# Kernel optimization log

Measured on AMD Instinct MI355X. Metric: run time of the kernel, lower is better.

The kernel has to match this reference:

```python
import jax, jax.numpy as jnp
import numpy as np

N_LAYER = 3
N_HEAD = 12
D_K = 64
D_V = 64
D_MODEL = 768
D_INNER = 4096
LN_EPS = 1e-5
BN_EPS = 1e-5
PAD_ID = 1


def _layernorm(x, g, b):
    m = jnp.mean(x, axis=-1, keepdims=True)
    v = jnp.mean((x - m) ** 2, axis=-1, keepdims=True)
    return g * (x - m) / jnp.sqrt(v + LN_EPS) + b


def _batchnorm(x, g, b):
    # training-mode BatchNorm1d: per-feature batch statistics
    m = jnp.mean(x, axis=0)
    v = jnp.mean((x - m) ** 2, axis=0)
    return g * (x - m) / jnp.sqrt(v + BN_EPS) + b


def setup_inputs() -> dict:
    key = jax.random.key(0)
    ks = jax.random.split(key, 24)
    B, C, S, H = 4, 4, 256, D_MODEL
    inp = {
        'input_ids': jax.random.randint(ks[0], (B, C, S), 0, 50000, dtype=jnp.int64) if jax.config.read('jax_enable_x64') else jax.random.randint(ks[0], (B, C, S), 0, 50000, dtype=jnp.int32),
        'roberta_attn': jax.random.normal(ks[1], (B, C, S, H), dtype=jnp.float32),
        'pooled_output': jax.random.normal(ks[2], (B * C, H), dtype=jnp.float32),
        'commonsense_mask': jax.random.uniform(ks[3], (B, C, S, S), dtype=jnp.float32),
        'dependency_mask': jax.random.uniform(ks[4], (B, C, S, S), dtype=jnp.float32),
        'entity_mask': jax.random.uniform(ks[5], (B, C, S), dtype=jnp.float32),
        'sentiment_mask': jax.random.uniform(ks[6], (B, C, S, S), dtype=jnp.float32),
    }
    s = 0.02
    inp['lin_w'] = s * jax.random.normal(ks[7], (H, N_LAYER * 4), dtype=jnp.float32)
    inp['lin_b'] = jnp.zeros((N_LAYER * 4,), jnp.float32)
    inp['Wq'] = s * jax.random.normal(ks[8], (N_LAYER, H, N_HEAD * D_K), dtype=jnp.float32)
    inp['bq'] = jnp.zeros((N_LAYER, N_HEAD * D_K), jnp.float32)
    inp['Wk'] = s * jax.random.normal(ks[9], (N_LAYER, H, N_HEAD * D_K), dtype=jnp.float32)
    inp['bk'] = jnp.zeros((N_LAYER, N_HEAD * D_K), jnp.float32)
    inp['Wv'] = s * jax.random.normal(ks[10], (N_LAYER, H, N_HEAD * D_V), dtype=jnp.float32)
    inp['bv'] = jnp.zeros((N_LAYER, N_HEAD * D_V), jnp.float32)
    inp['Wo'] = s * jax.random.normal(ks[11], (N_LAYER, N_HEAD * D_V, H), dtype=jnp.float32)
    inp['bo'] = jnp.zeros((N_LAYER, H), jnp.float32)
    inp['ln1_g'] = jnp.ones((N_LAYER, H), jnp.float32)
    inp['ln1_b'] = jnp.zeros((N_LAYER, H), jnp.float32)
    inp['W1'] = s * jax.random.normal(ks[12], (N_LAYER, H, D_INNER), dtype=jnp.float32)
    inp['b1'] = jnp.zeros((N_LAYER, D_INNER), jnp.float32)
    inp['W2'] = s * jax.random.normal(ks[13], (N_LAYER, D_INNER, H), dtype=jnp.float32)
    inp['b2'] = jnp.zeros((N_LAYER, H), jnp.float32)
    inp['ln2_g'] = jnp.ones((N_LAYER, H), jnp.float32)
    inp['ln2_b'] = jnp.zeros((N_LAYER, H), jnp.float32)
    inp['bnt_g'] = jnp.ones((H,), jnp.float32)
    inp['bnt_b'] = jnp.zeros((H,), jnp.float32)
    inp['pool_w'] = s * jax.random.normal(ks[14], (H, H), dtype=jnp.float32)
    inp['pool_b'] = jnp.zeros((H,), jnp.float32)
    inp['bn_g'] = jnp.ones((H,), jnp.float32)
    inp['bn_b'] = jnp.zeros((H,), jnp.float32)
    inp['cls_w'] = s * jax.random.normal(ks[15], (H, 1), dtype=jnp.float32)
    inp['cls_b'] = jnp.zeros((1,), jnp.float32)
    return inp


def reference(input_ids, roberta_attn, pooled_output, commonsense_mask, dependency_mask,
              entity_mask, sentiment_mask, lin_w, lin_b, Wq, bq, Wk, bk, Wv, bv, Wo, bo,
              ln1_g, ln1_b, W1, b1, W2, b2, ln2_g, ln2_b, bnt_g, bnt_b,
              pool_w, pool_b, bn_g, bn_b, cls_w, cls_b):
    B, C, S = input_ids.shape
    H = roberta_attn.shape[-1]
    N = B * C
    x = roberta_attn.reshape(N, S, H)

    # learned softmax fusion weights over the 4 relational masks, per layer
    w = jnp.mean(x, axis=1) @ lin_w + lin_b                       # [N, 3*4]
    w = jax.nn.softmax(w.reshape(N, N_LAYER, 4).transpose(1, 0, 2), axis=-1)  # [3, N, 4]

    ent = jnp.broadcast_to(entity_mask[:, :, None, :], (B, C, S, S))
    masks = jnp.stack([
        commonsense_mask.reshape(N, S, S),
        dependency_mask.reshape(N, S, S),
        ent.reshape(N, S, S),
        sentiment_mask.reshape(N, S, S),
    ], axis=1)                                                     # [N, 4, S, S]
    bias = jnp.einsum('lnm,nmqk->lnqk', w, masks)                  # [3, N, S, S]

    non_pad = (input_ids.reshape(N, S) != PAD_ID).astype(x.dtype)[:, :, None]  # [N, S, 1]

    enc = x
    scale = 1.0 / np.sqrt(D_K).astype(np.float32)
    for l in range(N_LAYER):
        residual = enc
        q = (enc @ Wq[l] + bq[l]).reshape(N, S, N_HEAD, D_K)
        k = (enc @ Wk[l] + bk[l]).reshape(N, S, N_HEAD, D_K)
        v = (enc @ Wv[l] + bv[l]).reshape(N, S, N_HEAD, D_V)
        scores = jnp.einsum('nqhd,nkhd->nhqk', q, k) * scale + bias[l][:, None]  # [N,H,S,S]
        attn = jax.nn.softmax(scores, axis=-1)
        o = jnp.einsum('nhqk,nkhd->nqhd', attn, v).reshape(N, S, N_HEAD * D_V)
        o = o @ Wo[l] + bo[l]
        enc = _layernorm(o + residual, ln1_g[l], ln1_b[l]) * non_pad
        residual = enc
        f = jax.nn.relu(enc @ W1[l] + b1[l]) @ W2[l] + b2[l]
        enc = _layernorm(f + residual, ln2_g[l], ln2_b[l]) * non_pad

    enc = _batchnorm(enc.reshape(N * S, H), bnt_g, bnt_b).reshape(N, S, H)
    seq = x + enc
    pooled = jnp.tanh(seq[:, 0] @ pool_w + pool_b)
    pooled = _batchnorm(pooled, bn_g, bn_b)
    logits = pooled @ cls_w + cls_b                                # [N, 1]
    return logits.reshape(-1, C)
```

## Files before the change

### kernel.cpp

```cpp
#include <hip/hip_runtime.h>
#include <hip/hip_bf16.h>
#include <math.h>

#define NSEQ 16
#define SEQ 256
#define H 768
#define NH 12
#define DKH 64
#define DI 4096
#define MROWS (NSEQ*SEQ)
#define QKVN (3*H)

typedef __bf16 v8bf __attribute__((ext_vector_type(8)));
typedef float  v4f  __attribute__((ext_vector_type(4)));
typedef short  v8s  __attribute__((ext_vector_type(8)));

__device__ inline unsigned short bf16b(float f) {
  __hip_bfloat16 h = __float2bfloat16(f);
  return *reinterpret_cast<unsigned short*>(&h);
}
__device__ inline float b2f(unsigned short b) {
  return __uint_as_float(((unsigned int)b) << 16);
}

__device__ __forceinline__ void gload16(const void* g, void* l) {
  __builtin_amdgcn_global_load_lds((const __attribute__((address_space(1))) void*)g,
                                   (__attribute__((address_space(3))) void*)l, 16, 0, 0);
}

__device__ __forceinline__ void waitvm(int n) {
  switch (n) {
    case 0:  asm volatile("s_waitcnt vmcnt(0)" ::: "memory"); break;
    case 4:  asm volatile("s_waitcnt vmcnt(4)" ::: "memory"); break;
    case 8:  asm volatile("s_waitcnt vmcnt(8)" ::: "memory"); break;
    case 12: asm volatile("s_waitcnt vmcnt(12)" ::: "memory"); break;
    case 16: asm volatile("s_waitcnt vmcnt(16)" ::: "memory"); break;
    default: asm volatile("s_waitcnt vmcnt(0)" ::: "memory"); break;
  }
}

enum { MODE_F32_BIAS=0, MODE_BF16_BIAS=1, MODE_BF16_BIAS_RELU=2, MODE_SCORES=3, MODE_PV=4, MODE_F32_NOBIAS=5 };

template<int BM, int BN, int MODE, int DEPTH, bool SWZ>
__global__ __launch_bounds__(256) void k_mm(
    const unsigned short* __restrict__ A, int lda, long long saN, long long saH,
    const unsigned short* __restrict__ B, int ldb, long long sbN, long long sbH,
    void* __restrict__ Cout, int ldc, long long scN, long long scH,
    const float* __restrict__ bias, int K, int nhdiv) {
  constexpr int MI = BM/32, NI = BN/32;
  constexpr int AISS = BM/32, BISS = BN/32;
  constexpr int LPT = AISS + BISS;
  constexpr int TA = BM*64, TB = BN*64;
  __shared__ unsigned short As[DEPTH*TA];
  __shared__ unsigned short Bs[DEPTH*TB];
  int t = threadIdx.x;
  int z = blockIdx.z, n = z / nhdiv, h = z - n*nhdiv;
  int lane = t & 63, wid = t >> 6, wr = wid >> 1, wc = wid & 1;

  int bx = blockIdx.x, by = blockIdx.y;
  if (SWZ) {
    int gx = gridDim.x;
    int nwg = gx * gridDim.y;
    int lin = by*gx + bx;
    int q = nwg >> 3, r = nwg & 7;
    int xcd = lin & 7, idx = lin >> 3;
    int swz = (xcd < r) ? (xcd*(q+1) + idx) : (r*(q+1) + (xcd-r)*q + idx);
    bx = swz % gx; by = swz / gx;
  }

  const unsigned short* Ab = A + (size_t)n*saN + (size_t)h*saH + (size_t)by*BM*lda;
  const unsigned short* Bb = B + (size_t)n*sbN + (size_t)h*sbH + (size_t)bx*BN*ldb;

  const unsigned short* aSrc[AISS]; int aOff[AISS];
#pragma unroll
  for (int r = 0; r < AISS; ++r) {
    int chunk = wid*AISS + r;
    int row = chunk*8 + (lane >> 3);
    int col = ((lane & 7) ^ (row & 7)) * 8;
    aSrc[r] = Ab + (size_t)row*lda + col;
    aOff[r] = chunk*512;
  }
  const unsigned short* bSrc[BISS]; int bOff[BISS];
#pragma unroll
  for (int r = 0; r < BISS; ++r) {
    int chunk = wid*BISS + r;
    int row = chunk*8 + (lane >> 3);
    int col = ((lane & 7) ^ (row & 7)) * 8;
    bSrc[r] = Bb + (size_t)row*ldb + col;
    bOff[r] = chunk*512;
  }

  v4f acc[MI][NI];
#pragma unroll
  for (int i = 0; i < MI; ++i)
#pragma unroll
    for (int j = 0; j < NI; ++j) acc[i][j] = (v4f){0.f,0.f,0.f,0.f};

  auto issue = [&](int tt, int buf) {
    int k0 = tt << 6;
#pragma unroll
    for (int r = 0; r < AISS; ++r) gload16(aSrc[r] + k0, &As[buf*TA + aOff[r]]);
#pragma unroll
    for (int r = 0; r < BISS; ++r) gload16(bSrc[r] + k0, &Bs[buf*TB + bOff[r]]);
  };

  int nt = K >> 6;
  for (int p = 0; p < DEPTH-1 && p < nt; ++p) issue(p, p);
  int cbuf = 0;
  int ibuf = (DEPTH-1) % DEPTH;
  for (int tt = 0; tt < nt; ++tt) {
    int ahead = tt + DEPTH - 1;
    if (ahead < nt) {
      issue(ahead, ibuf);
      waitvm((DEPTH-1)*LPT);
    } else {
      waitvm((nt-1-tt)*LPT);
    }
    __builtin_amdgcn_s_barrier();
    asm volatile("" ::: "memory");
#pragma unroll
    for (int ks = 0; ks < 2; ++ks) {
      v8bf af[MI], bfr[NI];
#pragma unroll
      for (int i = 0; i < MI; ++i) {
        int row = wr*(BM/2) + i*16 + (lane & 15);
        int c = (ks*4 + (lane >> 4)) ^ (row & 7);
        af[i] = *(const v8bf*)&As[cbuf*TA + row*64 + c*8];
      }
#pragma unroll
      for (int j = 0; j < NI; ++j) {
        int row = wc*(BN/2) + j*16 + (lane & 15);
        int c = (ks*4 + (lane >> 4)) ^ (row & 7);
        bfr[j] = *(const v8bf*)&Bs[cbuf*TB + row*64 + c*8];
      }
#pragma unroll
      for (int i = 0; i < MI; ++i)
#pragma unroll
        for (int j = 0; j < NI; ++j)
          acc[i][j] = __builtin_amdgcn_mfma_f32_16x16x32_bf16(af[i], bfr[j], acc[i][j], 0, 0, 0);
    }
    asm volatile("s_waitcnt lgkmcnt(0)" ::: "memory");
    __builtin_amdgcn_s_barrier();
    asm volatile("" ::: "memory");
    cbuf = (cbuf + 1 == DEPTH) ? 0 : cbuf + 1;
    ibuf = (ibuf + 1 == DEPTH) ? 0 : ibuf + 1;
  }

  float* Cf = (float*)Cout;
  unsigned short* Ch = (unsigned short*)Cout;
  size_t cb = (size_t)n*scN + (size_t)h*scH;
  int grow0 = by*BM + wr*(BM/2);
  int gcol0 = bx*BN + wc*(BN/2);
#pragma unroll
  for (int i = 0; i < MI; ++i) {
#pragma unroll
    for (int j = 0; j < NI; ++j) {
      int col = gcol0 + j*16 + (lane & 15);
      float bval = 0.f;
      if (MODE == MODE_F32_BIAS || MODE == MODE_BF16_BIAS || MODE == MODE_BF16_BIAS_RELU)
        bval = bias[col];
#pragma unroll
      for (int r = 0; r < 4; ++r) {
        int row = grow0 + i*16 + (lane>>4)*4 + r;
        float v = acc[i][j][r];
        if (MODE == MODE_F32_BIAS) {
          Cf[cb + (size_t)row*ldc + col] = v + bval;
        } else if (MODE == MODE_F32_NOBIAS) {
          Cf[cb + (size_t)row*ldc + col] = v;
        } else if (MODE == MODE_PV) {
          Ch[cb + (size_t)row*ldc + col] = bf16b(v);
        } else {
          v += bval;
          if (MODE == MODE_BF16_BIAS_RELU) v = fmaxf(v, 0.f);
          Ch[cb + (size_t)row*ldc + col] = bf16b(v);
        }
      }
    }
  }
}

template<int MODE>
__global__ __launch_bounds__(512) void k_mm256(
    const unsigned short* __restrict__ A, int lda,
    const unsigned short* __restrict__ B, int ldb,
    void* __restrict__ Cout, int ldc,
    const float* __restrict__ bias, int K) {
  extern __shared__ __align__(16) unsigned short smem[];
  unsigned short* As = smem;
  unsigned short* Bs = smem + 2*16384;
  constexpr int TA = 256*64;
  int t = threadIdx.x, lane = t & 63, wid = t >> 6;
  int wr = wid >> 2, wc = wid & 3;

  int bx = blockIdx.x, by = blockIdx.y;
  {
    int gx = gridDim.x, nwg = gx * gridDim.y;
    int lin = by*gx + bx;
    int q = nwg >> 3, r = nwg & 7;
    int xcd = lin & 7, idx = lin >> 3;
    int swz = (xcd < r) ? (xcd*(q+1) + idx) : (r*(q+1) + (xcd-r)*q + idx);
    bx = swz % gx; by = swz / gx;
  }

  const unsigned short* Ab = A + (size_t)by*256*lda;
  const unsigned short* Bb = B + (size_t)bx*256*ldb;

  const unsigned short* aSrc[4]; int aOff[4];
  const unsigned short* bSrc[4]; int bOff[4];
#pragma unroll
  for (int r = 0; r < 4; ++r) {
    int chunk = wid*4 + r;
    int row = chunk*8 + (lane >> 3);
    int col = ((lane & 7) ^ (row & 7)) * 8;
    aSrc[r] = Ab + (size_t)row*lda + col;
    bSrc[r] = Bb + (size_t)row*ldb + col;
    aOff[r] = chunk*512;
    bOff[r] = chunk*512;
  }

  v4f acc[8][4];
#pragma unroll
  for (int i = 0; i < 8; ++i)
#pragma unroll
    for (int j = 0; j < 4; ++j) acc[i][j] = (v4f){0.f,0.f,0.f,0.f};

  auto issue = [&](int tt, int buf) {
    int k0 = tt << 6;
#pragma unroll
    for (int r = 0; r < 4; ++r) gload16(aSrc[r] + k0, &As[buf*TA + aOff[r]]);
#pragma unroll
    for (int r = 0; r < 4; ++r) gload16(bSrc[r] + k0, &Bs[buf*TA + bOff[r]]);
  };

  int nt = K >> 6;
  issue(0, 0);
  int cur = 0;
  for (int tt = 0; tt < nt; ++tt) {
    if (tt + 1 < nt) {
      issue(tt+1, cur^1);
      waitvm(8);
    } else {
      waitvm(0);
    }
    __builtin_amdgcn_s_barrier();
    asm volatile("" ::: "memory");
    __builtin_amdgcn_s_setprio(1);
#pragma unroll
    for (int ks = 0; ks < 2; ++ks) {
      v8bf af[8], bfr[4];
#pragma unroll
      for (int i = 0; i < 8; ++i) {
        int row = wr*128 + i*16 + (lane & 15);
        int c = (ks*4 + (lane >> 4)) ^ (row & 7);
        af[i] = *(const v8bf*)&As[cur*TA + row*64 + c*8];
      }
#pragma unroll
      for (int j = 0; j < 4; ++j) {
        int row = wc*64 + j*16 + (lane & 15);
        int c = (ks*4 + (lane >> 4)) ^ (row & 7);
        bfr[j] = *(const v8bf*)&Bs[cur*TA + row*64 + c*8];
      }
#pragma unroll
      for (int i = 0; i < 8; ++i)
#pragma unroll
        for (int j = 0; j < 4; ++j)
          acc[i][j] = __builtin_amdgcn_mfma_f32_16x16x32_bf16(af[i], bfr[j], acc[i][j], 0, 0, 0);
    }
    __builtin_amdgcn_s_setprio(0);
    asm volatile("s_waitcnt lgkmcnt(0)" ::: "memory");
    __builtin_amdgcn_s_barrier();
    asm volatile("" ::: "memory");
    cur ^= 1;
  }

  float* Cf = (float*)Cout;
  unsigned short* Ch = (unsigned short*)Cout;
  int grow0 = by*256 + wr*128;
  int gcol0 = bx*256 + wc*64;
#pragma unroll
  for (int i = 0; i < 8; ++i) {
#pragma unroll
    for (int j = 0; j < 4; ++j) {
      int col = gcol0 + j*16 + (lane & 15);
      float bval = 0.f;
      if (MODE == MODE_F32_BIAS || MODE == MODE_BF16_BIAS || MODE == MODE_BF16_BIAS_RELU)
        bval = bias[col];
#pragma unroll
      for (int r = 0; r < 4; ++r) {
        int row = grow0 + i*16 + (lane>>4)*4 + r;
        float v = acc[i][j][r];
        if (MODE == MODE_F32_BIAS) {
          Cf[(size_t)row*ldc + col] = v + bval;
        } else if (MODE == MODE_F32_NOBIAS) {
          Cf[(size_t)row*ldc + col] = v;
        } else {
          v += bval;
          if (MODE == MODE_BF16_BIAS_RELU) v = fmaxf(v, 0.f);
          Ch[(size_t)row*ldc + col] = bf16b(v);
        }
      }
    }
  }
}

__global__ __launch_bounds__(256) void k_qksm(
    const unsigned short* __restrict__ qkv,
    const float* __restrict__ biasb,
    unsigned short* __restrict__ P) {
  __shared__ unsigned short Qs[64*64];
  __shared__ unsigned short Ks[256*64];
  int t = threadIdx.x, lane = t & 63, wid = t >> 6;
  int z = blockIdx.y, n = z / NH, h = z - n*NH;
  int m0 = blockIdx.x * 64;
  const unsigned short* Qb = qkv + (size_t)n*SEQ*QKVN + (size_t)h*DKH + (size_t)m0*QKVN;
  const unsigned short* Kb = qkv + (size_t)n*SEQ*QKVN + H + (size_t)h*DKH;
#pragma unroll
  for (int r = 0; r < 2; ++r) {
    int chunk = wid*2 + r;
    int row = chunk*8 + (lane >> 3);
    int col = ((lane & 7) ^ (row & 7)) * 8;
    gload16(Qb + (size_t)row*QKVN + col, &Qs[chunk*512]);
  }
#pragma unroll
  for (int r = 0; r < 8; ++r) {
    int chunk = wid*8 + r;
    int row = chunk*8 + (lane >> 3);
    int col = ((lane & 7) ^ (row & 7)) * 8;
    gload16(Kb + (size_t)row*QKVN + col, &Ks[chunk*512]);
  }
  __syncthreads();
  v4f acc[16];
#pragma unroll
  for (int j = 0; j < 16; ++j) acc[j] = (v4f){0.f,0.f,0.f,0.f};
#pragma unroll
  for (int ks = 0; ks < 2; ++ks) {
    int arow = wid*16 + (lane & 15);
    int ac = (ks*4 + (lane >> 4)) ^ (arow & 7);
    v8bf af = *(const v8bf*)&Qs[arow*64 + ac*8];
#pragma unroll
    for (int j = 0; j < 16; ++j) {
      int brow = j*16 + (lane & 15);
      int bc = (ks*4 + (lane >> 4)) ^ (brow & 7);
      v8bf bf = *(const v8bf*)&Ks[brow*64 + bc*8];
      acc[j] = __builtin_amdgcn_mfma_f32_16x16x32_bf16(af, bf, acc[j], 0, 0, 0);
    }
  }
  int col = lane & 15, quad = lane >> 4;
  const float* bb = biasb + (size_t)n*65536;
  float e[16][4];
  float rm[4] = {-1e30f, -1e30f, -1e30f, -1e30f};
#pragma unroll
  for (int r = 0; r < 4; ++r) {
    int row = m0 + wid*16 + quad*4 + r;
#pragma unroll
    for (int j = 0; j < 16; ++j) {
      float v = acc[j][r]*0.125f + bb[(size_t)row*256 + j*16 + col];
      e[j][r] = v;
      rm[r] = fmaxf(rm[r], v);
    }
  }
#pragma unroll
  for (int r = 0; r < 4; ++r)
#pragma unroll
    for (int m = 1; m < 16; m <<= 1) rm[r] = fmaxf(rm[r], __shfl_xor(rm[r], m, 64));
  float rs[4] = {0.f, 0.f, 0.f, 0.f};
#pragma unroll
  for (int r = 0; r < 4; ++r)
#pragma unroll
    for (int j = 0; j < 16; ++j) {
      float ev = __expf(e[j][r] - rm[r]);
      e[j][r] = ev;
      rs[r] += ev;
    }
#pragma unroll
  for (int r = 0; r < 4; ++r) {
#pragma unroll
    for (int m = 1; m < 16; m <<= 1) rs[r] += __shfl_xor(rs[r], m, 64);
    rs[r] = 1.0f/rs[r];
  }
  unsigned short* Pz = P + (size_t)z*65536;
#pragma unroll
  for (int r = 0; r < 4; ++r) {
    int row = m0 + wid*16 + quad*4 + r;
#pragma unroll
    for (int j = 0; j < 16; ++j)
      Pz[(size_t)row*256 + j*16 + col] = bf16b(e[j][r]*rs[r]);
  }
}

__global__ __launch_bounds__(256) void k_wT(const float* __restrict__ in,
                                            unsigned short* __restrict__ out,
                                            int Nn, int Kk) {
  int n0 = blockIdx.x*64, k0 = blockIdx.y*64;
  __shared__ float T[64][72];
  int t = threadIdx.x;
  int r = t >> 4, c4 = (t & 15) * 4;
#pragma unroll
  for (int i = 0; i < 4; ++i) {
    float4 v = *(const float4*)(in + (size_t)(k0 + r + i*16)*Nn + n0 + c4);
    T[c4+0][r+i*16] = v.x; T[c4+1][r+i*16] = v.y;
    T[c4+2][r+i*16] = v.z; T[c4+3][r+i*16] = v.w;
  }
  __syncthreads();
  int c = t >> 3, r8 = (t & 7) * 8;
#pragma unroll
  for (int i = 0; i < 2; ++i) {
    int cc = c + i*32;
    v8s o;
#pragma unroll
    for (int j = 0; j < 8; ++j) o[j] = (short)bf16b(T[cc][r8+j]);
    *(v8s*)(out + (size_t)(n0+cc)*Kk + k0 + r8) = o;
  }
}

__global__ void k_bqkv(const float* __restrict__ bq, const float* __restrict__ bk,
                       const float* __restrict__ bv, float* __restrict__ o) {
  int i = blockIdx.x*256 + threadIdx.x;
  if (i >= 3*QKVN) return;
  int l = i / QKVN, j = i - l*QKVN;
  float v = (j < H) ? bq[l*H + j] : (j < 2*H) ? bk[l*H + j - H] : bv[l*H + j - 2*H];
  o[i] = v;
}

__global__ __launch_bounds__(256) void k_cast(const float* __restrict__ x,
                                              float* __restrict__ enc,
                                              unsigned short* __restrict__ enc16) {
  size_t i = ((size_t)blockIdx.x*256 + threadIdx.x)*4;
  float4 v = *(const float4*)(x + i);
  *(float4*)(enc + i) = v;
  ushort4 u = { bf16b(v.x), bf16b(v.y), bf16b(v.z), bf16b(v.w) };
  *(ushort4*)(enc16 + i) = u;
}

__global__ __launch_bounds__(256) void k_vT(const unsigned short* __restrict__ qkv,
                                            unsigned short* __restrict__ vT) {
  int z = blockIdx.x, n = z/NH, h = z - n*NH;
  const unsigned short* src = qkv + (size_t)n*SEQ*QKVN + 2*H + (size_t)h*DKH;
  __shared__ unsigned short tile[64][264];
  int t = threadIdx.x;
  int r0 = t >> 3, d0 = (t & 7) * 8;
#pragma unroll
  for (int i = 0; i < 8; ++i) {
    int r = r0 + i*32;
    v8s vv = *(const v8s*)(src + (size_t)r*QKVN + d0);
#pragma unroll
    for (int j = 0; j < 8; ++j) tile[d0+j][r] = (unsigned short)vv[j];
  }
  __syncthreads();
  int d = t >> 2, rb = (t & 3) * 64;
  unsigned short* dst = vT + (size_t)z*DKH*SEQ + (size_t)d*SEQ + rb;
#pragma unroll
  for (int i = 0; i < 8; ++i)
    *(v8s*)(dst + i*8) = *(const v8s*)&tile[d][rb + i*8];
}

__global__ __launch_bounds__(256) void k_fusion_weights(
    const float* __restrict__ x, const float* __restrict__ lin_w,
    const float* __restrict__ lin_b, float* __restrict__ wsoft) {
  int n = blockIdx.x, t = threadIdx.x;
  __shared__ float xm[H];
  __shared__ float sred[4];
  __shared__ float logits[12];
  if (t < 192) {
    const float4* p = (const float4*)(x + (size_t)n*SEQ*H) + t;
    float4 s = {0.f,0.f,0.f,0.f};
    for (int r = 0; r < SEQ; ++r) {
      float4 v = p[(size_t)r*192];
      s.x += v.x; s.y += v.y; s.z += v.z; s.w += v.w;
    }
    xm[t*4+0] = s.x*(1.0f/SEQ); xm[t*4+1] = s.y*(1.0f/SEQ);
    xm[t*4+2] = s.z*(1.0f/SEQ); xm[t*4+3] = s.w*(1.0f/SEQ);
  }
  __syncthreads();
  float lacc[12];
#pragma unroll
  for (int j = 0; j < 12; ++j) lacc[j] = 0.f;
  for (int hh = t; hh < H; hh += 256) {
    float xv = xm[hh];
#pragma unroll
    for (int j = 0; j < 12; ++j) lacc[j] += xv * lin_w[hh*12 + j];
  }
  for (int j = 0; j < 12; ++j) {
    float v = lacc[j];
#pragma unroll
    for (int m = 1; m < 64; m <<= 1) v += __shfl_xor(v, m, 64);
    if ((t & 63) == 0) sred[t >> 6] = v;
    __syncthreads();
    if (t == 0) logits[j] = sred[0]+sred[1]+sred[2]+sred[3] + lin_b[j];
    __syncthreads();
  }
  if (t < 3) {
    int l = t;
    float mx = -1e30f;
    for (int m = 0; m < 4; ++m) mx = fmaxf(mx, logits[l*4+m]);
    float e[4], s = 0.f;
    for (int m = 0; m < 4; ++m) { e[m] = expf(logits[l*4+m]-mx); s += e[m]; }
    for (int m = 0; m < 4; ++m) wsoft[(l*NSEQ + n)*4 + m] = e[m]/s;
  }
}

__global__ __launch_bounds__(256) void k_bias(
    const float* __restrict__ cm, const float* __restrict__ dm,
    const float* __restrict__ ent, const float* __restrict__ sm,
    const float* __restrict__ wsoft, int l, float* __restrict__ bias) {
  int g = blockIdx.x*256 + threadIdx.x;
  int n = g >> 14;
  int k4 = g & 63;
  const float* w = wsoft + (l*NSEQ + n)*4;
  float w0 = w[0], w1 = w[1], w2 = w[2], w3 = w[3];
  float4 c = ((const float4*)cm)[g];
  float4 d = ((const float4*)dm)[g];
  float4 s = ((const float4*)sm)[g];
  float4 e = ((const float4*)(ent + (size_t)n*SEQ))[k4];
  float4 o;
  o.x = w0*c.x + w1*d.x + w2*e.x + w3*s.x;
  o.y = w0*c.y + w1*d.y + w2*e.y + w3*s.y;
  o.z = w0*c.z + w1*d.z + w2*e.z + w3*s.z;
  o.w = w0*c.w + w1*d.w + w2*e.w + w3*s.w;
  ((float4*)bias)[g] = o;
}

__global__ void k_nonpad(const int* __restrict__ ids, float* __restrict__ npad) {
  int i = blockIdx.x*256 + threadIdx.x;
  if (i < MROWS) npad[i] = (ids[i] != 1) ? 1.0f : 0.0f;
}

__global__ __launch_bounds__(256) void k_ln(
    const float* __restrict__ f, float* __restrict__ enc,
    unsigned short* __restrict__ enc16,
    const float* __restrict__ g, const float* __restrict__ b,
    const float* __restrict__ npad) {
  int r = blockIdx.x, t = threadIdx.x;
  size_t base = (size_t)r*H;
  float v0 = f[base+t]     + enc[base+t];
  float v1 = f[base+t+256] + enc[base+t+256];
  float v2 = f[base+t+512] + enc[base+t+512];
  __shared__ float sred[4];
  float s = v0+v1+v2;
#pragma unroll
  for (int m = 1; m < 64; m <<= 1) s += __shfl_xor(s, m, 64);
  if ((t & 63) == 0) sred[t >> 6] = s;
  __syncthreads();
  float mean = (sred[0]+sred[1]+sred[2]+sred[3]) * (1.0f/H);
  __syncthreads();
  float d0 = v0-mean, d1 = v1-mean, d2 = v2-mean;
  float ss = d0*d0 + d1*d1 + d2*d2;
#pragma unroll
  for (int m = 1; m < 64; m <<= 1) ss += __shfl_xor(ss, m, 64);
  if ((t & 63) == 0) sred[t >> 6] = ss;
  __syncthreads();
  float var = (sred[0]+sred[1]+sred[2]+sred[3]) * (1.0f/H);
  float rstd = 1.0f/sqrtf(var + 1e-5f);
  float npv = npad[r];
  float o0 = (g[t]    *d0*rstd + b[t]    )*npv;
  float o1 = (g[t+256]*d1*rstd + b[t+256])*npv;
  float o2 = (g[t+512]*d2*rstd + b[t+512])*npv;
  enc[base+t]     = o0; enc[base+t+256] = o1; enc[base+t+512] = o2;
  enc16[base+t]     = bf16b(o0);
  enc16[base+t+256] = bf16b(o1);
  enc16[base+t+512] = bf16b(o2);
}

__global__ __launch_bounds__(256) void k_ln4(
    const float* __restrict__ p, float* __restrict__ enc,
    unsigned short* __restrict__ enc16,
    const float* __restrict__ g, const float* __restrict__ b,
    const float* __restrict__ npad, const float* __restrict__ cbias) {
  int r = blockIdx.x, t = threadIdx.x;
  size_t base = (size_t)r*H;
  const size_t PS = (size_t)MROWS*H;
  float v0 = p[base+t]     + p[PS+base+t]     + p[2*PS+base+t]     + p[3*PS+base+t]     + cbias[t]     + enc[base+t];
  float v1 = p[base+t+256] + p[PS+base+t+256] + p[2*PS+base+t+256] + p[3*PS+base+t+256] + cbias[t+256] + enc[base+t+256];
  float v2 = p[base+t+512] + p[PS+base+t+512] + p[2*PS+base+t+512] + p[3*PS+base+t+512] + cbias[t+512] + enc[base+t+512];
  __shared__ float sred[4];
  float s = v0+v1+v2;
#pragma unroll
  for (int m = 1; m < 64; m <<= 1) s += __shfl_xor(s, m, 64);
  if ((t & 63) == 0) sred[t >> 6] = s;
  __syncthreads();
  float mean = (sred[0]+sred[1]+sred[2]+sred[3]) * (1.0f/H);
  __syncthreads();
  float d0 = v0-mean, d1 = v1-mean, d2 = v2-mean;
  float ss = d0*d0 + d1*d1 + d2*d2;
#pragma unroll
  for (int m = 1; m < 64; m <<= 1) ss += __shfl_xor(ss, m, 64);
  if ((t & 63) == 0) sred[t >> 6] = ss;
  __syncthreads();
  float var = (sred[0]+sred[1]+sred[2]+sred[3]) * (1.0f/H);
  float rstd = 1.0f/sqrtf(var + 1e-5f);
  float npv = npad[r];
  float o0 = (g[t]    *d0*rstd + b[t]    )*npv;
  float o1 = (g[t+256]*d1*rstd + b[t+256])*npv;
  float o2 = (g[t+512]*d2*rstd + b[t+512])*npv;
  enc[base+t]     = o0; enc[base+t+256] = o1; enc[base+t+512] = o2;
  enc16[base+t]     = bf16b(o0);
  enc16[base+t+256] = bf16b(o1);
  enc16[base+t+512] = bf16b(o2);
}

__global__ __launch_bounds__(256) void k_colstats(
    const float* __restrict__ enc, float* __restrict__ csum, float* __restrict__ csq) {
  int r0 = blockIdx.x*64, t = threadIdx.x;
  float s0=0,s1=0,s2=0,q0=0,q1=0,q2=0;
  for (int r = 0; r < 64; ++r) {
    const float* row = enc + (size_t)(r0+r)*H;
    float a = row[t], b = row[t+256], c = row[t+512];
    s0 += a; s1 += b; s2 += c;
    q0 += a*a; q1 += b*b; q2 += c*c;
  }
  atomicAdd(&csum[t],     s0); atomicAdd(&csum[t+256], s1); atomicAdd(&csum[t+512], s2);
  atomicAdd(&csq[t],      q0); atomicAdd(&csq[t+256],  q1); atomicAdd(&csq[t+512],  q2);
}

__global__ __launch_bounds__(256) void k_poolprep(
    const float* __restrict__ x, const float* __restrict__ enc,
    const float* __restrict__ csum, const float* __restrict__ csq,
    const float* __restrict__ bnt_g, const float* __restrict__ bnt_b,
    float* __restrict__ ps0) {
  int n = blockIdx.x, t = threadIdx.x;
  for (int hh = t; hh < H; hh += 256) {
    float m = csum[hh] * (1.0f/MROWS);
    float var = csq[hh] * (1.0f/MROWS) - m*m;
    float rstd = 1.0f/sqrtf(var + 1e-5f);
    float e = enc[(size_t)n*SEQ*H + hh];
    ps0[n*H + hh] = x[(size_t)n*SEQ*H + hh] + bnt_g[hh]*(e-m)*rstd + bnt_b[hh];
  }
}

__global__ __launch_bounds__(256) void k_poolmm(
    const float* __restrict__ ps0, const float* __restrict__ pool_w,
    const float* __restrict__ pool_b, float* __restrict__ pooled) {
  int n = blockIdx.y, jb = blockIdx.x*64;
  __shared__ float s0[H];
  __shared__ float part[4][64];
  int t = threadIdx.x;
  for (int hh = t; hh < H; hh += 256) s0[hh] = ps0[n*H + hh];
  __syncthreads();
  int j = t & 63, q = t >> 6;
  float a = 0.f;
  int h0 = q*192;
  for (int hh = h0; hh < h0+192; ++hh)
    a = fmaf(s0[hh], pool_w[(size_t)hh*H + jb + j], a);
  part[q][j] = a;
  __syncthreads();
  if (t < 64) {
    float v = part[0][t]+part[1][t]+part[2][t]+part[3][t] + pool_b[jb+t];
    pooled[n*H + jb + t] = tanhf(v);
  }
}

__global__ __launch_bounds__(256) void k_final(
    const float* __restrict__ pooled, const float* __restrict__ bn_g,
    const float* __restrict__ bn_b, const float* __restrict__ cls_w,
    const float* __restrict__ cls_b, float* __restrict__ out) {
  int t = threadIdx.x;
  float acc[16];
#pragma unroll
  for (int n = 0; n < 16; ++n) acc[n] = 0.f;
  for (int hh = t; hh < H; hh += 256) {
    float p[16]; float m = 0.f;
#pragma unroll
    for (int n = 0; n < 16; ++n) { p[n] = pooled[n*H + hh]; m += p[n]; }
    m *= (1.0f/16.f);
    float var = 0.f;
#pragma unroll
    for (int n = 0; n < 16; ++n) { float d = p[n]-m; var += d*d; }
    var *= (1.0f/16.f);
    float rstd = 1.0f/sqrtf(var + 1e-5f);
    float gw = bn_g[hh]*rstd*cls_w[hh];
    float off = bn_b[hh]*cls_w[hh];
#pragma unroll
    for (int n = 0; n < 16; ++n) acc[n] += (p[n]-m)*gw + off;
  }
  __shared__ float sred[4];
  for (int n = 0; n < 16; ++n) {
    float v = acc[n];
#pragma unroll
    for (int m = 1; m < 64; m <<= 1) v += __shfl_xor(v, m, 64);
    if ((t & 63) == 0) sred[t >> 6] = v;
    __syncthreads();
    if (t == 0) out[n] = sred[0]+sred[1]+sred[2]+sred[3] + cls_b[0];
    __syncthreads();
  }
}

extern "C" void kernel_launch(void* const* d_in, const int* in_sizes, int n_in,
                              void* d_out, int out_size, void* d_ws, size_t ws_size,
                              hipStream_t stream) {
  const int*   input_ids = (const int*)  d_in[0];
  const float* x       = (const float*)d_in[1];
  const float* cm      = (const float*)d_in[3];
  const float* dm      = (const float*)d_in[4];
  const float* ent     = (const float*)d_in[5];
  const float* sm      = (const float*)d_in[6];
  const float* lin_w   = (const float*)d_in[7];
  const float* lin_b   = (const float*)d_in[8];
  const float* Wq      = (const float*)d_in[9];
  const float* bq      = (const float*)d_in[10];
  const float* Wk      = (const float*)d_in[11];
  const float* bk      = (const float*)d_in[12];
  const float* Wv      = (const float*)d_in[13];
  const float* bv      = (const float*)d_in[14];
  const float* Wo      = (const float*)d_in[15];
  const float* bo      = (const float*)d_in[16];
  const float* ln1_g   = (const float*)d_in[17];
  const float* ln1_b   = (const float*)d_in[18];
  const float* W1      = (const float*)d_in[19];
  const float* b1      = (const float*)d_in[20];
  const float* W2      = (const float*)d_in[21];
  const float* b2      = (const float*)d_in[22];
  const float* ln2_g   = (const float*)d_in[23];
  const float* ln2_b   = (const float*)d_in[24];
  const float* bnt_g   = (const float*)d_in[25];
  const float* bnt_b   = (const float*)d_in[26];
  const float* pool_w  = (const float*)d_in[27];
  const float* pool_b  = (const float*)d_in[28];
  const float* bn_g    = (const float*)d_in[29];
  const float* bn_b    = (const float*)d_in[30];
  const float* cls_w   = (const float*)d_in[31];
  const float* cls_b   = (const float*)d_in[32];
  float* out = (float*)d_out;
  (void)ws_size; (void)n_in; (void)in_sizes; (void)out_size;

  char* wsb = (char*)d_ws;
  size_t off = 0;
  auto alloc = [&](size_t bytes) {
    void* p = (void*)(wsb + off);
    off += (bytes + 255) & ~(size_t)255;
    return p;
  };
  float* enc            = (float*)alloc((size_t)MROWS*H*4);
  unsigned short* enc16 = (unsigned short*)alloc((size_t)MROWS*H*2);
  unsigned short* qkv16 = (unsigned short*)alloc((size_t)MROWS*QKVN*2);
  unsigned short* vT    = (unsigned short*)alloc((size_t)192*DKH*SEQ*2);
  unsigned short* ob16  = (unsigned short*)alloc((size_t)MROWS*H*2);
  float* fbuf           = (float*)alloc((size_t)4*MROWS*H*4);
  unsigned short* PH    = (unsigned short*)alloc((size_t)MROWS*DI*2);
  unsigned short* P16     = PH;
  unsigned short* hidden16 = PH;
  float* biasb          = (float*)alloc((size_t)NSEQ*SEQ*SEQ*4);
  unsigned short* WqkvT = (unsigned short*)alloc((size_t)3*QKVN*H*2);
  unsigned short* WoT   = (unsigned short*)alloc((size_t)3*H*H*2);
  unsigned short* W1T   = (unsigned short*)alloc((size_t)3*DI*H*2);
  unsigned short* W2T   = (unsigned short*)alloc((size_t)3*H*DI*2);
  float* bqkv   = (float*)alloc(3*QKVN*4);
  float* wsoft  = (float*)alloc(3*16*4*4);
  float* npad   = (float*)alloc(MROWS*4);
  float* csum   = (float*)alloc(H*4);
  float* csq    = (float*)alloc(H*4);
  float* ps0    = (float*)alloc(16*H*4);
  float* pooled = (float*)alloc(16*H*4);

  k_cast<<<MROWS*H/1024, 256, 0, stream>>>(x, enc, enc16);
  k_fusion_weights<<<16, 256, 0, stream>>>(x, lin_w, lin_b, wsoft);
  k_nonpad<<<MROWS/256, 256, 0, stream>>>(input_ids, npad);
  k_bqkv<<<27, 256, 0, stream>>>(bq, bk, bv, bqkv);
  for (int l = 0; l < 3; ++l) {
    k_wT<<<dim3(12,12), 256, 0, stream>>>(Wq + (size_t)l*H*H, WqkvT + (size_t)l*QKVN*H,           H, H);
    k_wT<<<dim3(12,12), 256, 0, stream>>>(Wk + (size_t)l*H*H, WqkvT + (size_t)l*QKVN*H + H*H,     H, H);
    k_wT<<<dim3(12,12), 256, 0, stream>>>(Wv + (size_t)l*H*H, WqkvT + (size_t)l*QKVN*H + 2*H*H,   H, H);
    k_wT<<<dim3(12,12), 256, 0, stream>>>(Wo + (size_t)l*H*H, WoT + (size_t)l*H*H,                H, H);
    k_wT<<<dim3(64,12), 256, 0, stream>>>(W1 + (size_t)l*H*DI, W1T + (size_t)l*DI*H,              DI, H);
    k_wT<<<dim3(12,64), 256, 0, stream>>>(W2 + (size_t)l*DI*H, W2T + (size_t)l*H*DI,              H, DI);
  }

  for (int l = 0; l < 3; ++l) {
    k_bias<<<1024, 256, 0, stream>>>(cm, dm, ent, sm, wsoft, l, biasb);
    k_mm<128,128,MODE_BF16_BIAS,1,true><<<dim3(18,32,1), 256, 0, stream>>>(
        enc16, H, 0, 0, WqkvT + (size_t)l*QKVN*H, H, 0, 0,
        qkv16, QKVN, 0, 0, bqkv + l*QKVN, H, 1);
    k_qksm<<<dim3(4,192), 256, 0, stream>>>(qkv16, biasb, P16);
    k_vT<<<192, 256, 0, stream>>>(qkv16, vT);
    k_mm<64,64,MODE_PV,3,false><<<dim3(1,4,192), 256, 0, stream>>>(
        P16, SEQ, (long long)NH*SEQ*SEQ, (long long)SEQ*SEQ,
        vT, SEQ, (long long)NH*DKH*SEQ, (long long)DKH*SEQ,
        ob16, H, (long long)SEQ*H, DKH,
        nullptr, SEQ, NH);
    k_mm<64,64,MODE_F32_BIAS,3,true><<<dim3(12,64,1), 256, 0, stream>>>(
        ob16, H, 0, 0, WoT + (size_t)l*H*H, H, 0, 0,
        fbuf, H, 0, 0, bo + l*H, H, 1);
    k_ln<<<MROWS, 256, 0, stream>>>(fbuf, enc, enc16, ln1_g + l*H, ln1_b + l*H, npad);
    k_mm256<MODE_BF16_BIAS_RELU><<<dim3(16,16), 512, 131072, stream>>>(
        enc16, H, W1T + (size_t)l*DI*H, H, hidden16, DI, b1 + l*DI, H);
    k_mm<128,128,MODE_F32_NOBIAS,2,true><<<dim3(6,32,4), 256, 0, stream>>>(
        hidden16, DI, 0, 1024, W2T + (size_t)l*H*DI, DI, 0, 1024,
        fbuf, H, 0, (long long)MROWS*H, nullptr, 1024, 4);
    k_ln4<<<MROWS, 256, 0, stream>>>(fbuf, enc, enc16, ln2_g + l*H, ln2_b + l*H, npad, b2 + l*H);
  }

  hipMemsetAsync(csum, 0, H*sizeof(float), stream);
  hipMemsetAsync(csq,  0, H*sizeof(float), stream);
  k_colstats<<<64, 256, 0, stream>>>(enc, csum, csq);
  k_poolprep<<<16, 256, 0, stream>>>(x, enc, csum, csq, bnt_g, bnt_b, ps0);
  k_poolmm<<<dim3(12,16), 256, 0, stream>>>(ps0, pool_w, pool_b, pooled);
  k_final<<<1, 256, 0, stream>>>(pooled, bn_g, bn_b, cls_w, cls_b, out);
}
```

Baseline: 658.6 us.

## Store attention bias in bf16, add BK template to GEMM, widen colstats grid

Attention bias is now stored as bf16 instead of fp32, which halves the memory traffic for writing and reading the bias tensor in each layer. The GEMM kernel gains a BK template parameter: the QKV and W2 GEMMs move to BK=32, and the QKV GEMM goes from one pipeline stage to two, with a matching swizzle and vmcnt(2) wait. Column statistics use four times more blocks with fewer rows each, for more parallelism. Rounding the bias to bf16 adds a small precision loss in the attention scores.

```diff
diff --git a/kernel.cpp b/kernel.cpp
--- a/kernel.cpp
+++ b/kernel.cpp
@@ -31,6 +31,7 @@
 __device__ __forceinline__ void waitvm(int n) {
   switch (n) {
     case 0:  asm volatile("s_waitcnt vmcnt(0)" ::: "memory"); break;
+    case 2:  asm volatile("s_waitcnt vmcnt(2)" ::: "memory"); break;
     case 4:  asm volatile("s_waitcnt vmcnt(4)" ::: "memory"); break;
     case 8:  asm volatile("s_waitcnt vmcnt(8)" ::: "memory"); break;
     case 12: asm volatile("s_waitcnt vmcnt(12)" ::: "memory"); break;
@@ -41,16 +42,20 @@
 
 enum { MODE_F32_BIAS=0, MODE_BF16_BIAS=1, MODE_BF16_BIAS_RELU=2, MODE_SCORES=3, MODE_PV=4, MODE_F32_NOBIAS=5 };
 
-template<int BM, int BN, int MODE, int DEPTH, bool SWZ>
+template<int BM, int BN, int MODE, int BK, int DEPTH, bool SWZ>
 __global__ __launch_bounds__(256) void k_mm(
     const unsigned short* __restrict__ A, int lda, long long saN, long long saH,
     const unsigned short* __restrict__ B, int ldb, long long sbN, long long sbH,
     void* __restrict__ Cout, int ldc, long long scN, long long scH,
     const float* __restrict__ bias, int K, int nhdiv) {
   constexpr int MI = BM/32, NI = BN/32;
-  constexpr int AISS = BM/32, BISS = BN/32;
+  constexpr int CH  = BK/8;
+  constexpr int RPC = 512/BK;
+  constexpr int SW  = CH - 1;
+  constexpr int SSH = (BK == 32) ? 1 : 0;
+  constexpr int AISS = BM*BK/2048, BISS = BN*BK/2048;
   constexpr int LPT = AISS + BISS;
-  constexpr int TA = BM*64, TB = BN*64;
+  constexpr int TA = BM*BK, TB = BN*BK;
   __shared__ unsigned short As[DEPTH*TA];
   __shared__ unsigned short Bs[DEPTH*TB];
   int t = threadIdx.x;
@@ -75,8 +80,8 @@
 #pragma unroll
   for (int r = 0; r < AISS; ++r) {
     int chunk = wid*AISS + r;
-    int row = chunk*8 + (lane >> 3);
-    int col = ((lane & 7) ^ (row & 7)) * 8;
+    int row = chunk*RPC + lane/CH;
+    int col = ((lane % CH) ^ ((row >> SSH) & SW)) * 8;
     aSrc[r] = Ab + (size_t)row*lda + col;
     aOff[r] = chunk*512;
   }
@@ -84,8 +89,8 @@
 #pragma unroll
   for (int r = 0; r < BISS; ++r) {
     int chunk = wid*BISS + r;
-    int row = chunk*8 + (lane >> 3);
-    int col = ((lane & 7) ^ (row & 7)) * 8;
+    int row = chunk*RPC + lane/CH;
+    int col = ((lane % CH) ^ ((row >> SSH) & SW)) * 8;
     bSrc[r] = Bb + (size_t)row*ldb + col;
     bOff[r] = chunk*512;
   }
@@ -97,14 +102,14 @@
     for (int j = 0; j < NI; ++j) acc[i][j] = (v4f){0.f,0.f,0.f,0.f};
 
   auto issue = [&](int tt, int buf) {
-    int k0 = tt << 6;
+    int k0 = tt * BK;
 #pragma unroll
     for (int r = 0; r < AISS; ++r) gload16(aSrc[r] + k0, &As[buf*TA + aOff[r]]);
 #pragma unroll
     for (int r = 0; r < BISS; ++r) gload16(bSrc[r] + k0, &Bs[buf*TB + bOff[r]]);
   };
 
-  int nt = K >> 6;
+  int nt = K / BK;
   for (int p = 0; p < DEPTH-1 && p < nt; ++p) issue(p, p);
   int cbuf = 0;
   int ibuf = (DEPTH-1) % DEPTH;
@@ -119,19 +124,19 @@
     __builtin_amdgcn_s_barrier();
     asm volatile("" ::: "memory");
 #pragma unroll
-    for (int ks = 0; ks < 2; ++ks) {
+    for (int ks = 0; ks < BK/32; ++ks) {
       v8bf af[MI], bfr[NI];
 #pragma unroll
       for (int i = 0; i < MI; ++i) {
         int row = wr*(BM/2) + i*16 + (lane & 15);
-        int c = (ks*4 + (lane >> 4)) ^ (row & 7);
-        af[i] = *(const v8bf*)&As[cbuf*TA + row*64 + c*8];
+        int c = (ks*4 + (lane >> 4)) ^ ((row >> SSH) & SW);
+        af[i] = *(const v8bf*)&As[cbuf*TA + row*BK + c*8];
       }
 #pragma unroll
       for (int j = 0; j < NI; ++j) {
         int row = wc*(BN/2) + j*16 + (lane & 15);
-        int c = (ks*4 + (lane >> 4)) ^ (row & 7);
-        bfr[j] = *(const v8bf*)&Bs[cbuf*TB + row*64 + c*8];
+        int c = (ks*4 + (lane >> 4)) ^ ((row >> SSH) & SW);
+        bfr[j] = *(const v8bf*)&Bs[cbuf*TB + row*BK + c*8];
       }
 #pragma unroll
       for (int i = 0; i < MI; ++i)
@@ -305,7 +310,7 @@
 
 __global__ __launch_bounds__(256) void k_qksm(
     const unsigned short* __restrict__ qkv,
-    const float* __restrict__ biasb,
+    const unsigned short* __restrict__ biasb,
     unsigned short* __restrict__ P) {
   __shared__ unsigned short Qs[64*64];
   __shared__ unsigned short Ks[256*64];
@@ -346,7 +351,7 @@
     }
   }
   int col = lane & 15, quad = lane >> 4;
-  const float* bb = biasb + (size_t)n*65536;
+  const unsigned short* bb = biasb + (size_t)n*65536;
   float e[16][4];
   float rm[4] = {-1e30f, -1e30f, -1e30f, -1e30f};
 #pragma unroll
@@ -354,7 +359,7 @@
     int row = m0 + wid*16 + quad*4 + r;
 #pragma unroll
     for (int j = 0; j < 16; ++j) {
-      float v = acc[j][r]*0.125f + bb[(size_t)row*256 + j*16 + col];
+      float v = acc[j][r]*0.125f + b2f(bb[(size_t)row*256 + j*16 + col]);
       e[j][r] = v;
       rm[r] = fmaxf(rm[r], v);
     }
@@ -502,7 +507,7 @@
 __global__ __launch_bounds__(256) void k_bias(
     const float* __restrict__ cm, const float* __restrict__ dm,
     const float* __restrict__ ent, const float* __restrict__ sm,
-    const float* __restrict__ wsoft, int l, float* __restrict__ bias) {
+    const float* __restrict__ wsoft, int l, unsigned short* __restrict__ bias) {
   int g = blockIdx.x*256 + threadIdx.x;
   int n = g >> 14;
   int k4 = g & 63;
@@ -512,12 +517,12 @@
   float4 d = ((const float4*)dm)[g];
   float4 s = ((const float4*)sm)[g];
   float4 e = ((const float4*)(ent + (size_t)n*SEQ))[k4];
-  float4 o;
-  o.x = w0*c.x + w1*d.x + w2*e.x + w3*s.x;
-  o.y = w0*c.y + w1*d.y + w2*e.y + w3*s.y;
-  o.z = w0*c.z + w1*d.z + w2*e.z + w3*s.z;
-  o.w = w0*c.w + w1*d.w + w2*e.w + w3*s.w;
-  ((float4*)bias)[g] = o;
+  ushort4 o;
+  o.x = bf16b(w0*c.x + w1*d.x + w2*e.x + w3*s.x);
+  o.y = bf16b(w0*c.y + w1*d.y + w2*e.y + w3*s.y);
+  o.z = bf16b(w0*c.z + w1*d.z + w2*e.z + w3*s.z);
+  o.w = bf16b(w0*c.w + w1*d.w + w2*e.w + w3*s.w);
+  ((ushort4*)bias)[g] = o;
 }
 
 __global__ void k_nonpad(const int* __restrict__ ids, float* __restrict__ npad) {
@@ -600,9 +605,9 @@
 
 __global__ __launch_bounds__(256) void k_colstats(
     const float* __restrict__ enc, float* __restrict__ csum, float* __restrict__ csq) {
-  int r0 = blockIdx.x*64, t = threadIdx.x;
+  int r0 = blockIdx.x*16, t = threadIdx.x;
   float s0=0,s1=0,s2=0,q0=0,q1=0,q2=0;
-  for (int r = 0; r < 64; ++r) {
+  for (int r = 0; r < 16; ++r) {
     const float* row = enc + (size_t)(r0+r)*H;
     float a = row[t], b = row[t+256], c = row[t+512];
     s0 += a; s1 += b; s2 += c;
@@ -738,7 +743,7 @@
   unsigned short* PH    = (unsigned short*)alloc((size_t)MROWS*DI*2);
   unsigned short* P16     = PH;
   unsigned short* hidden16 = PH;
-  float* biasb          = (float*)alloc((size_t)NSEQ*SEQ*SEQ*4);
+  unsigned short* biasb = (unsigned short*)alloc((size_t)NSEQ*SEQ*SEQ*2);
   unsigned short* WqkvT = (unsigned short*)alloc((size_t)3*QKVN*H*2);
   unsigned short* WoT   = (unsigned short*)alloc((size_t)3*H*H*2);
   unsigned short* W1T   = (unsigned short*)alloc((size_t)3*DI*H*2);
@@ -766,23 +771,23 @@
 
   for (int l = 0; l < 3; ++l) {
     k_bias<<<1024, 256, 0, stream>>>(cm, dm, ent, sm, wsoft, l, biasb);
-    k_mm<128,128,MODE_BF16_BIAS,1,true><<<dim3(18,32,1), 256, 0, stream>>>(
+    k_mm<128,128,MODE_BF16_BIAS,32,2,true><<<dim3(18,32,1), 256, 0, stream>>>(
         enc16, H, 0, 0, WqkvT + (size_t)l*QKVN*H, H, 0, 0,
         qkv16, QKVN, 0, 0, bqkv + l*QKVN, H, 1);
     k_qksm<<<dim3(4,192), 256, 0, stream>>>(qkv16, biasb, P16);
     k_vT<<<192, 256, 0, stream>>>(qkv16, vT);
-    k_mm<64,64,MODE_PV,3,false><<<dim3(1,4,192), 256, 0, stream>>>(
+    k_mm<64,64,MODE_PV,64,3,false><<<dim3(1,4,192), 256, 0, stream>>>(
         P16, SEQ, (long long)NH*SEQ*SEQ, (long long)SEQ*SEQ,
         vT, SEQ, (long long)NH*DKH*SEQ, (long long)DKH*SEQ,
         ob16, H, (long long)SEQ*H, DKH,
         nullptr, SEQ, NH);
-    k_mm<64,64,MODE_F32_BIAS,3,true><<<dim3(12,64,1), 256, 0, stream>>>(
+    k_mm<64,64,MODE_F32_BIAS,64,3,true><<<dim3(12,64,1), 256, 0, stream>>>(
         ob16, H, 0, 0, WoT + (size_t)l*H*H, H, 0, 0,
         fbuf, H, 0, 0, bo + l*H, H, 1);
     k_ln<<<MROWS, 256, 0, stream>>>(fbuf, enc, enc16, ln1_g + l*H, ln1_b + l*H, npad);
     k_mm256<MODE_BF16_BIAS_RELU><<<dim3(16,16), 512, 131072, stream>>>(
         enc16, H, W1T + (size_t)l*DI*H, H, hidden16, DI, b1 + l*DI, H);
-    k_mm<128,128,MODE_F32_NOBIAS,2,true><<<dim3(6,32,4), 256, 0, stream>>>(
+    k_mm<128,128,MODE_F32_NOBIAS,32,2,true><<<dim3(6,32,4), 256, 0, stream>>>(
         hidden16, DI, 0, 1024, W2T + (size_t)l*H*DI, DI, 0, 1024,
         fbuf, H, 0, (long long)MROWS*H, nullptr, 1024, 4);
     k_ln4<<<MROWS, 256, 0, stream>>>(fbuf, enc, enc16, ln2_g + l*H, ln2_b + l*H, npad, b2 + l*H);
@@ -790,7 +795,7 @@
 
   hipMemsetAsync(csum, 0, H*sizeof(float), stream);
   hipMemsetAsync(csq,  0, H*sizeof(float), stream);
-  k_colstats<<<64, 256, 0, stream>>>(enc, csum, csq);
+  k_colstats<<<256, 256, 0, stream>>>(enc, csum, csq);
   k_poolprep<<<16, 256, 0, stream>>>(x, enc, csum, csq, bnt_g, bnt_b, ps0);
   k_poolmm<<<dim3(12,16), 256, 0, stream>>>(ps0, pool_w, pool_b, pooled);
   k_final<<<1, 256, 0, stream>>>(pooled, bn_g, bn_b, cls_w, cls_b, out);
```

After: 643.4 us. 1.02x faster.
